# Kernel optimization log

Measured on AMD Instinct MI355X. Metric: run time of the kernel, lower is better.

The kernel has to match this reference:

```python
import jax, jax.numpy as jnp
import numpy as np

VOC, EDIM, HDIM, SSZ, SDIM, SDEPTH, PAD = 32000, 256, 256, 128, 128, 2, 0
N, BSZ = 64, 32
T = 2 * N - 1  # 127
N_ACTS = 2  # push, pop


def _linear(key, out_d, in_d):
    k1, k2 = jax.random.split(key)
    return (jax.random.normal(k1, (out_d, in_d), jnp.float32) * 0.02,
            jax.random.normal(k2, (out_d,), jnp.float32) * 0.02)


def setup_inputs() -> dict:
    key = jax.random.key(0)
    ks = jax.random.split(key, 9)
    emb_W = jax.random.normal(ks[0], (VOC, EDIM), jnp.float32) * 0.02
    emb_W = emb_W.at[PAD].set(0.0)  # padding_idx row is zero in torch
    W_e2h, b_e2h = _linear(ks[1], HDIM, EDIM)
    W_s2h, b_s2h = _linear(ks[2], HDIM, SDIM * SDEPTH)
    W_h2h, b_h2h = _linear(ks[3], HDIM, HDIM)
    W_h2i, b_h2i = _linear(ks[4], N_ACTS + 1, HDIM)
    W_h2s, b_h2s = _linear(ks[5], SDIM, HDIM)
    W_s2u, b_s2u = _linear(ks[6], SDIM, SDIM * SDEPTH)
    empty_elem = jax.random.normal(ks[7], (1, SDIM), jnp.float32) * 0.02
    inputs = jax.random.randint(ks[8], (N, BSZ), 0, VOC)
    return dict(inputs=inputs, emb_W=emb_W, W_e2h=W_e2h, b_e2h=b_e2h,
                W_s2h=W_s2h, b_s2h=b_s2h, W_h2h=W_h2h, b_h2h=b_h2h,
                W_h2i=W_h2i, b_h2i=b_h2i, W_h2s=W_h2s, b_h2s=b_h2s,
                W_s2u=W_s2u, b_s2u=b_s2u, empty_elem=empty_elem)


def _srnn(inputs, emb_W, W_e2h, b_e2h, W_s2h, b_s2h, W_h2h, b_h2h,
          W_h2i, b_h2i, W_h2s, b_h2s, W_s2u, b_s2u, empty_elem):
    bsz = inputs.shape[1]
    embs = emb_W[inputs]                                        # [N, bsz, edim]
    pads = jnp.broadcast_to(emb_W[PAD], (T - N, bsz, EDIM))     # padded tail
    buf0 = jnp.concatenate([embs, pads], axis=0)                # [T, bsz, edim]
    hid0 = jnp.zeros((bsz, HDIM), jnp.float32)
    stack0 = jnp.broadcast_to(empty_elem, (bsz, SSZ, SDIM))

    def step(carry, t):
        hid, stack, buf = carry
        tops = stack[:, :SDEPTH, :].reshape(bsz, SDEPTH * SDIM)
        inp = buf[t]                                            # [bsz, edim]
        ihid = inp @ W_e2h.T + b_e2h + tops @ W_s2h.T + b_s2h
        hid = jax.nn.relu(hid @ W_h2h.T + b_h2h + ihid)
        inst = ihid @ W_h2i.T + b_h2i                           # [bsz, 3]
        act = jax.nn.softmax(inst[:, :N_ACTS], axis=-1)
        gamma = 1.0 + jnp.log1p(jnp.exp(inst[:, N_ACTS:]))      # [bsz, 1]
        a = act ** gamma
        a = a / (jnp.sum(a, axis=-1, keepdims=True) + 1e-16)    # sharpened acts
        p_push, p_pop = a[:, :1], a[:, 1:]                      # [bsz, 1]
        # buffer update: pop shifts the whole buffer down one slot along time
        buf_pop = jnp.concatenate([jnp.zeros_like(buf[:1]), buf[:-1]], axis=0)
        buf = p_push[None] * buf + p_pop[None] * buf_pop        # [1,bsz,1] bcast
        push_val = jax.nn.relu(hid @ W_h2s.T + b_h2s)           # [bsz, sdim]
        u_val = jax.nn.relu(tops @ W_s2u.T + b_s2u)             # [bsz, sdim]
        z = jnp.zeros((bsz, 1, SDIM), jnp.float32)
        # W_push (shift down by 1) as an index roll
        stack_push = jnp.concatenate([z, stack[:, :-1, :]], axis=1)
        stack_push = stack_push.at[:, 0, :].add(push_val)
        # W_pop = shift up by SDEPTH, then W_push = shift down by 1
        up = jnp.concatenate([stack[:, SDEPTH:, :],
                              jnp.zeros((bsz, SDEPTH, SDIM), jnp.float32)], axis=1)
        stack_pop = jnp.concatenate([z, up[:, :-1, :]], axis=1)
        stack_pop = stack_pop.at[:, 0, :].add(u_val)
        stack_pop = stack_pop.at[:, SSZ - SDEPTH + 1:, :].add(empty_elem[0])
        stack = p_push[:, :, None] * stack_push + p_pop[:, :, None] * stack_pop
        return (hid, stack, buf), (hid, a, stack[:, 0, :])

    (hid, stack, _), (outputs, acts, top_elems) = jax.lax.scan(
        step, (hid0, stack0, buf0), jnp.arange(T))
    return outputs, hid, stack, acts, top_elems


def reference(inputs, emb_W, W_e2h, b_e2h, W_s2h, b_s2h, W_h2h, b_h2h,
              W_h2i, b_h2i, W_h2s, b_h2s, W_s2u, b_s2u, empty_elem):
    return _srnn(inputs, emb_W, W_e2h, b_e2h, W_s2h, b_s2h, W_h2h, b_h2h,
                 W_h2i, b_h2i, W_h2s, b_h2s, W_s2u, b_s2u, empty_elem)
```

## Files before the change

kernel.cpp:

```cpp
#include <hip/hip_runtime.h>
#include <stdint.h>
#include <math.h>


#define T_STEPS 127

#define OUT_OFF   0
#define HID_OFF   1040384
#define STACK_OFF 1048576
#define ACTS_OFF  1572864
#define TE_OFF    1580992

#define E2H_OFF_U 131072

typedef _Float16 h2 __attribute__((ext_vector_type(2)));

__device__ __forceinline__ unsigned packh2(float a, float b){
  h2 v; v.x = (_Float16)a; v.y = (_Float16)b;
  return __builtin_bit_cast(unsigned, v);
}
__device__ __forceinline__ float h2loF(unsigned u){ h2 v = __builtin_bit_cast(h2,u); return (float)v.x; }
__device__ __forceinline__ float h2hiF(unsigned u){ h2 v = __builtin_bit_cast(h2,u); return (float)v.y; }

#if __has_builtin(__builtin_amdgcn_fdot2)
__device__ __forceinline__ float fdot2(unsigned a, unsigned b, float c){
  return __builtin_amdgcn_fdot2(__builtin_bit_cast(h2,a), __builtin_bit_cast(h2,b), c, false);
}
#else
__device__ __forceinline__ float fdot2(unsigned a, unsigned b, float c){
  return c + h2loF(a)*h2loF(b) + h2hiF(a)*h2hiF(b);
}
#endif

#define CHOFF(u) (12*((u)>>3) + ((u)&7))

__global__ void prep_pack(const float* __restrict__ We2h, const float* __restrict__ Ws2h,
                          const float* __restrict__ Wh2h, const float* __restrict__ Wh2s,
                          const float* __restrict__ Ws2u, uint4* __restrict__ out4){
  int gid = blockIdx.x*256 + threadIdx.x;
  const float* src;
  if (gid < 16384){
    int i = gid >> 10, t_ = gid & 1023;
    const float* S = (t_ < 512) ? Ws2h : Wh2h;
    int r = t_ & 511, jp = r >> 2, ks = r & 3;
    int j = 2*jp + (i >> 3);
    int k0 = ks*64 + (i & 7)*8;
    src = S + j*256 + k0;
  } else if (gid < 20480){
    int l = gid - 16384, i = l >> 10, t_ = l & 1023;
    int jr = t_ >> 4, kb = t_ & 15;
    int j = 2*jr + (i >> 1);
    int k0 = kb*16 + (i & 1)*8;
    src = Wh2s + j*256 + k0;
  } else if (gid < 24576){
    int l = gid - 20480, i = l >> 10, t_ = l & 1023;
    int jr = t_ >> 4, kb = t_ & 15;
    int j = 2*jr + (i >> 1);
    int k0 = kb*16 + (i & 1)*8;
    src = Ws2u + j*256 + k0;
  } else {
    int l = gid - 24576;
    int i8 = l >> 8, j = l & 255;
    src = We2h + j*256 + i8*8;
  }
  uint4 r4;
  r4.x = packh2(src[0], src[1]); r4.y = packh2(src[2], src[3]);
  r4.z = packh2(src[4], src[5]); r4.w = packh2(src[6], src[7]);
  out4[gid] = r4;
}

__global__ void prep_e2h(const int* __restrict__ inputs, const float* __restrict__ embW,
                         const uint4* __restrict__ w04, unsigned* __restrict__ e2hpk){
  __shared__ float emb[8][256];
  int tid = threadIdx.x;
  int r2 = blockIdx.x >> 3, bg = blockIdx.x & 7;
  for (int q=0;q<8;q++){
    int rr = q >> 2, bb = q & 3;
    int tok = inputs[(2*r2+rr)*32 + bg*4+bb];
    emb[q][tid] = embW[tok*256 + tid];
  }
  __syncthreads();
  float acc[8] = {0.f,0.f,0.f,0.f,0.f,0.f,0.f,0.f};
  for (int i8=0;i8<32;i8++){
    uint4 u = w04[i8*256 + tid];
    unsigned uu[4] = {u.x,u.y,u.z,u.w};
    #pragma unroll
    for (int c=0;c<4;c++){
      float lo = h2loF(uu[c]), hi = h2hiF(uu[c]);
      int k = i8*8 + c*2;
      #pragma unroll
      for (int q=0;q<8;q++)
        acc[q] += emb[q][k]*lo + emb[q][k+1]*hi;
    }
  }
  int base = (bg*4)*8192 + r2*256 + tid;
  #pragma unroll
  for (int bb=0;bb<4;bb++)
    e2hpk[base + bb*8192] = packh2(acc[bb], acc[4+bb]);
}

__global__ __attribute__((amdgpu_flat_work_group_size(1024,1024), amdgpu_waves_per_eu(4,4)))
void srnn_main(const uint4* __restrict__ ws4, const unsigned* __restrict__ wsu,
               const float* __restrict__ b_e2h, const float* __restrict__ b_s2h,
               const float* __restrict__ b_h2h, const float* __restrict__ Wh2i,
               const float* __restrict__ b_h2i, const float* __restrict__ b_h2s,
               const float* __restrict__ b_s2u, const float* __restrict__ empty_el,
               float* __restrict__ out)
{
  __shared__ __align__(16) float    stk_s[128*128];
  __shared__ __align__(16) unsigned e2h_s[32*258];
  __shared__ __align__(16) unsigned s_pk[192];
  __shared__ __align__(16) unsigned hid_pk[192];
  __shared__ __align__(16) float    pv_s[128], uv_s[128];
  __shared__ __align__(16) float    accih[256], acchp[256];
  __shared__ __align__(16) float    emptyf_s[128];
  __shared__ float    wbuf[2][192];
  __shared__ unsigned pkwc[32];
  __shared__ float    partsum[12];
  __shared__ float    pp_s, pq_s;

  const int tid = threadIdx.x;
  const int b   = blockIdx.x;
  const int aside = tid >> 9;
  const int ar  = tid & 511;
  const int ajp = ar >> 2;
  const int aks = ar & 3;
  const int jr  = tid >> 4;
  const int ksb = tid & 15;
  const int g   = tid >> 6;
  const int cp  = tid & 63;

  uint4 w1r[16], w3r[4], w2r[4];
  #pragma unroll
  for (int i=0;i<16;i++) w1r[i] = ws4[i*1024 + tid];
  #pragma unroll
  for (int i=0;i<4;i++)  w3r[i] = ws4[16384 + i*1024 + tid];
  #pragma unroll
  for (int i=0;i<4;i++)  w2r[i] = ws4[20480 + i*1024 + tid];

  float bA0=0.f, bA1=0.f;
  if (aks==0){
    int j0 = 2*ajp;
    if (aside==0){ bA0 = b_e2h[j0]+b_s2h[j0]; bA1 = b_e2h[j0+1]+b_s2h[j0+1]; }
    else         { bA0 = b_h2h[j0];           bA1 = b_h2h[j0+1]; }
  }
  float bH0=0.f,bH1=0.f,bU0=0.f,bU1=0.f;
  if (ksb==0){ bH0=b_h2s[2*jr]; bH1=b_h2s[2*jr+1]; bU0=b_s2u[2*jr]; bU1=b_s2u[2*jr+1]; }
  float rW0=0.f,rW1=0.f,rW2=0.f;
  if (tid<256){ rW0=Wh2i[tid]; rW1=Wh2i[256+tid]; rW2=Wh2i[512+tid]; }
  const float bi0=b_h2i[0], bi1=b_h2i[1], bi2=b_h2i[2];

  const unsigned* e2hg = wsu + E2H_OFF_U + b*8192;
  #pragma unroll
  for (int q=0;q<8;q++){
    int idx = q*1024 + tid;
    e2h_s[(idx>>8)*258 + (idx&255)] = e2hg[idx];
  }
  {
    float2 e2 = *(const float2*)&empty_el[2*cp];
    #pragma unroll
    for (int j=0;j<8;j++)
      *(float2*)&stk_s[(8*g+j)*128 + 2*cp] = e2;
  }
  if (tid < 128){
    emptyf_s[tid] = empty_el[tid];
    hid_pk[CHOFF(tid)] = 0u;
    int cu = tid & 63;
    s_pk[CHOFF(tid)] = packh2(empty_el[2*cu], empty_el[2*cu+1]);
  }
  if (tid < 192){ wbuf[0][tid] = (tid==64)?1.f:0.f; wbuf[1][tid]=0.f; }
  if (tid < 32)  pkwc[tid] = (tid==0)? packh2(1.f,0.f) : 0u;
  __syncthreads();

  int cur = 0;
  for (int t=0;t<T_STEPS;++t){
    {
      const unsigned* act  = aside ? hid_pk : s_pk;
      const unsigned* actB = act + 48*aks;
      float x0 = 0.f, x1 = 0.f;
      if (aside==0){
        #pragma unroll
        for (int q=0;q<8;q++){
          int r2 = aks*8 + q;
          unsigned cw = pkwc[r2];
          uint2 e = *(const uint2*)&e2h_s[r2*258 + 2*ajp];
          x0 = fdot2(cw, e.x, x0);
          x1 = fdot2(cw, e.y, x1);
        }
      }
      #pragma unroll
      for (int i=0;i<8;i++){
        uint4 A  = *(const uint4*)(actB + 12*(i>>1) + 4*(i&1));
        uint4 Wa = w1r[i], Wb = w1r[8+i];
        x0 = fdot2(A.x,Wa.x,x0); x0 = fdot2(A.y,Wa.y,x0);
        x0 = fdot2(A.z,Wa.z,x0); x0 = fdot2(A.w,Wa.w,x0);
        x1 = fdot2(A.x,Wb.x,x1); x1 = fdot2(A.y,Wb.y,x1);
        x1 = fdot2(A.z,Wb.z,x1); x1 = fdot2(A.w,Wb.w,x1);
      }
      x0 += __shfl_xor(x0,1); x0 += __shfl_xor(x0,2);
      x1 += __shfl_xor(x1,1); x1 += __shfl_xor(x1,2);
      if (aks==0){
        float* dst = aside ? acchp : accih;
        *(float2*)&dst[2*ajp] = make_float2(x0 + bA0, x1 + bA1);
      }
    }
    __syncthreads();

    if (tid < 128){
      float2 ih2 = *(const float2*)&accih[2*tid];
      float2 hp2 = *(const float2*)&acchp[2*tid];
      float hn0 = fmaxf(ih2.x+hp2.x, 0.f);
      float hn1 = fmaxf(ih2.y+hp2.y, 0.f);
      hid_pk[CHOFF(tid)] = packh2(hn0,hn1);
      *(float2*)&out[OUT_OFF + t*8192 + b*256 + 2*tid] = make_float2(hn0,hn1);
      if (t==T_STEPS-1) *(float2*)&out[HID_OFF + b*256 + 2*tid] = make_float2(hn0,hn1);
    }
    if (tid < 256){
      float v = accih[tid];
      float p0=v*rW0, p1=v*rW1, p2=v*rW2;
      #pragma unroll
      for (int o=32;o>=1;o>>=1){ p0+=__shfl_xor(p0,o); p1+=__shfl_xor(p1,o); p2+=__shfl_xor(p2,o); }
      if ((tid&63)==0){ int w=tid>>6; partsum[w*3]=p0; partsum[w*3+1]=p1; partsum[w*3+2]=p2; }
    }
    __syncthreads();

    if (tid < 64){
      float i0 = bi0+partsum[0]+partsum[3]+partsum[6]+partsum[9];
      float i1 = bi1+partsum[1]+partsum[4]+partsum[7]+partsum[10];
      float gi = bi2+partsum[2]+partsum[5]+partsum[8]+partsum[11];
      float mx = fmaxf(i0,i1);
      float e0 = expf(i0-mx), e1 = expf(i1-mx);
      float inv = 1.f/(e0+e1);
      float act0 = e0*inv, act1 = e1*inv;
      float gamma = 1.f + log1pf(expf(gi));
      float A0 = powf(act0,gamma), A1 = powf(act1,gamma);
      float sden = A0+A1+1e-16f;
      float ppv = A0/sden, pqv = A1/sden;
      if (tid==0){
        pp_s = ppv; pq_s = pqv;
        *(float2*)&out[ACTS_OFF + t*64 + b*2] = make_float2(ppv,pqv);
      }
    }

    {
      const uint4* hptr = (const uint4*)(hid_pk + 12*ksb);
      const uint4* sptr = (const uint4*)(s_pk   + 12*ksb);
      uint4 H0 = hptr[0], H1 = hptr[1];
      uint4 S0 = sptr[0], S1 = sptr[1];
      float h0=0.f,h1=0.f,u0=0.f,u1=0.f;
      h0=fdot2(H0.x,w3r[0].x,h0); h0=fdot2(H0.y,w3r[0].y,h0); h0=fdot2(H0.z,w3r[0].z,h0); h0=fdot2(H0.w,w3r[0].w,h0);
      h0=fdot2(H1.x,w3r[1].x,h0); h0=fdot2(H1.y,w3r[1].y,h0); h0=fdot2(H1.z,w3r[1].z,h0); h0=fdot2(H1.w,w3r[1].w,h0);
      h1=fdot2(H0.x,w3r[2].x,h1); h1=fdot2(H0.y,w3r[2].y,h1); h1=fdot2(H0.z,w3r[2].z,h1); h1=fdot2(H0.w,w3r[2].w,h1);
      h1=fdot2(H1.x,w3r[3].x,h1); h1=fdot2(H1.y,w3r[3].y,h1); h1=fdot2(H1.z,w3r[3].z,h1); h1=fdot2(H1.w,w3r[3].w,h1);
      u0=fdot2(S0.x,w2r[0].x,u0); u0=fdot2(S0.y,w2r[0].y,u0); u0=fdot2(S0.z,w2r[0].z,u0); u0=fdot2(S0.w,w2r[0].w,u0);
      u0=fdot2(S1.x,w2r[1].x,u0); u0=fdot2(S1.y,w2r[1].y,u0); u0=fdot2(S1.z,w2r[1].z,u0); u0=fdot2(S1.w,w2r[1].w,u0);
      u1=fdot2(S0.x,w2r[2].x,u1); u1=fdot2(S0.y,w2r[2].y,u1); u1=fdot2(S0.z,w2r[2].z,u1); u1=fdot2(S0.w,w2r[2].w,u1);
      u1=fdot2(S1.x,w2r[3].x,u1); u1=fdot2(S1.y,w2r[3].y,u1); u1=fdot2(S1.z,w2r[3].z,u1); u1=fdot2(S1.w,w2r[3].w,u1);
      #pragma unroll
      for (int o=8;o>=1;o>>=1){
        h0+=__shfl_xor(h0,o); h1+=__shfl_xor(h1,o);
        u0+=__shfl_xor(u0,o); u1+=__shfl_xor(u1,o);
      }
      if (ksb==0){
        pv_s[2*jr]   = fmaxf(h0+bH0,0.f);
        pv_s[2*jr+1] = fmaxf(h1+bH1,0.f);
        uv_s[2*jr]   = fmaxf(u0+bU0,0.f);
        uv_s[2*jr+1] = fmaxf(u1+bU1,0.f);
      }
    }
    __syncthreads();
    const float pp = pp_s, pq = pq_s;

    {
      float2 w[10];
      #pragma unroll
      for (int k=0;k<10;k++){
        int r = 8*g - 1 + k;
        if (r >= 0 && r <= 127)
          w[k] = *(const float2*)&stk_s[r*128 + 2*cp];
      }
      if (g == 15) w[9] = *(const float2*)&emptyf_s[2*cp];
      float2 pv2 = make_float2(0.f,0.f), uv2 = make_float2(0.f,0.f);
      if (g == 0){ pv2 = *(const float2*)&pv_s[2*cp]; uv2 = *(const float2*)&uv_s[2*cp]; }
      float2 nn[8];
      #pragma unroll
      for (int j=0;j<8;j++){
        nn[j].x = pp*w[j].x + pq*w[j+2].x;
        nn[j].y = pp*w[j].y + pq*w[j+2].y;
      }
      if (g == 0){
        nn[0].x = pp*pv2.x + pq*uv2.x;
        nn[0].y = pp*pv2.y + pq*uv2.y;
      }
      if (tid < 128){
        int k = 64+tid;
        wbuf[cur^1][k] = pp*wbuf[cur][k] + pq*wbuf[cur][k-1];
      } else if (tid < 160){
        int r2 = tid-128;
        int k1 = 65 + t - 2*r2;
        float wa = wbuf[cur][k1], wb2 = wbuf[cur][k1-1], wc2 = wbuf[cur][k1-2];
        pkwc[r2] = packh2(pp*wa+pq*wb2, pp*wb2+pq*wc2);
      }
      __syncthreads();
      #pragma unroll
      for (int j=0;j<8;j++)
        *(float2*)&stk_s[(8*g+j)*128 + 2*cp] = nn[j];
      if (g == 0){
        *(float2*)&out[TE_OFF + t*4096 + b*128 + 2*cp] = nn[0];
        s_pk[CHOFF(cp)]      = packh2(nn[0].x, nn[0].y);
        s_pk[CHOFF(64+cp)]   = packh2(nn[1].x, nn[1].y);
      }
    }
    __syncthreads();
    cur ^= 1;
  }

  #pragma unroll
  for (int j=0;j<8;j++){
    int r = 8*g + j;
    *(float2*)&out[STACK_OFF + b*16384 + r*128 + 2*cp] =
      *(const float2*)&stk_s[r*128 + 2*cp];
  }
}

extern "C" void kernel_launch(void* const* d_in, const int* in_sizes, int n_in,
                              void* d_out, int out_size, void* d_ws, size_t ws_size,
                              hipStream_t stream){
  const int*   inputs = (const int*)d_in[0];
  const float* embW   = (const float*)d_in[1];
  const float* We2h   = (const float*)d_in[2];
  const float* b_e2h  = (const float*)d_in[3];
  const float* Ws2h   = (const float*)d_in[4];
  const float* b_s2h  = (const float*)d_in[5];
  const float* Wh2h   = (const float*)d_in[6];
  const float* b_h2h  = (const float*)d_in[7];
  const float* Wh2i   = (const float*)d_in[8];
  const float* b_h2i  = (const float*)d_in[9];
  const float* Wh2s   = (const float*)d_in[10];
  const float* b_h2s  = (const float*)d_in[11];
  const float* Ws2u   = (const float*)d_in[12];
  const float* b_s2u  = (const float*)d_in[13];
  const float* empty  = (const float*)d_in[14];
  unsigned* wsu = (unsigned*)d_ws;

  prep_pack<<<dim3(128), dim3(256), 0, stream>>>(We2h, Ws2h, Wh2h, Wh2s, Ws2u, (uint4*)wsu);
  prep_e2h<<<dim3(256), dim3(256), 0, stream>>>(inputs, embW, ((const uint4*)wsu)+24576, wsu + E2H_OFF_U);
  srnn_main<<<dim3(32), dim3(1024), 0, stream>>>((const uint4*)wsu, (const unsigned*)wsu,
                                                 b_e2h, b_s2h, b_h2h, Wh2i, b_h2i,
                                                 b_h2s, b_s2u, empty, (float*)d_out);
}
```

Measured before the change: 896.4 us.

## Halve block to 512 threads with more weights in registers per thread

The main recurrent kernel now runs with 512 threads per block instead of 1024. Each thread keeps twice as many packed fp16 weights in registers and does a longer dot-product chain with fewer shuffle reductions. The h2s and s2u projections are split across two thread halves, the weight packing layout is rewritten to match, and the padded CHOFF activation layout is dropped. The aim is to cut per-step barrier and shuffle cost in the serial 127-step loop, at the cost of higher register pressure and less parallelism per step.

```diff
diff --git a/kernel.cpp b/kernel.cpp
--- a/kernel.cpp
+++ b/kernel.cpp
@@ -31,8 +31,6 @@
   return c + h2loF(a)*h2loF(b) + h2hiF(a)*h2hiF(b);
 }
 #endif
-
-#define CHOFF(u) (12*((u)>>3) + ((u)&7))
 
 __global__ void prep_pack(const float* __restrict__ We2h, const float* __restrict__ Ws2h,
                           const float* __restrict__ Wh2h, const float* __restrict__ Wh2s,
@@ -40,24 +38,22 @@
   int gid = blockIdx.x*256 + threadIdx.x;
   const float* src;
   if (gid < 16384){
-    int i = gid >> 10, t_ = gid & 1023;
-    const float* S = (t_ < 512) ? Ws2h : Wh2h;
-    int r = t_ & 511, jp = r >> 2, ks = r & 3;
-    int j = 2*jp + (i >> 3);
-    int k0 = ks*64 + (i & 7)*8;
+    int i = gid >> 9, t_ = gid & 511;
+    int aside = t_ >> 8, ar = t_ & 255;
+    const float* S = aside ? Wh2h : Ws2h;
+    int ajp = ar >> 1, aks = ar & 1;
+    int j  = 2*ajp + (i >> 4);
+    int k0 = aks*128 + (i & 15)*8;
     src = S + j*256 + k0;
-  } else if (gid < 20480){
-    int l = gid - 16384, i = l >> 10, t_ = l & 1023;
-    int jr = t_ >> 4, kb = t_ & 15;
-    int j = 2*jr + (i >> 1);
-    int k0 = kb*16 + (i & 1)*8;
-    src = Wh2s + j*256 + k0;
   } else if (gid < 24576){
-    int l = gid - 20480, i = l >> 10, t_ = l & 1023;
-    int jr = t_ >> 4, kb = t_ & 15;
-    int j = 2*jr + (i >> 1);
-    int k0 = kb*16 + (i & 1)*8;
-    src = Ws2u + j*256 + k0;
+    int l = gid - 16384;
+    int i = l >> 9, t_ = l & 511;
+    int hside = t_ >> 8, r = t_ & 255;
+    const float* S = hside ? Ws2u : Wh2s;
+    int jr = r >> 2, ksb = r & 3;
+    int j  = 2*jr + (i >> 3);
+    int k0 = ksb*64 + (i & 7)*8;
+    src = S + j*256 + k0;
   } else {
     int l = gid - 24576;
     int i8 = l >> 8, j = l & 255;
@@ -99,7 +95,7 @@
     e2hpk[base + bb*8192] = packh2(acc[bb], acc[4+bb]);
 }
 
-__global__ __attribute__((amdgpu_flat_work_group_size(1024,1024), amdgpu_waves_per_eu(4,4)))
+__global__ __attribute__((amdgpu_flat_work_group_size(512,512), amdgpu_waves_per_eu(2,2)))
 void srnn_main(const uint4* __restrict__ ws4, const unsigned* __restrict__ wsu,
                const float* __restrict__ b_e2h, const float* __restrict__ b_s2h,
                const float* __restrict__ b_h2h, const float* __restrict__ Wh2i,
@@ -109,8 +105,8 @@
 {
   __shared__ __align__(16) float    stk_s[128*128];
   __shared__ __align__(16) unsigned e2h_s[32*258];
-  __shared__ __align__(16) unsigned s_pk[192];
-  __shared__ __align__(16) unsigned hid_pk[192];
+  __shared__ __align__(16) unsigned s_pk[128];
+  __shared__ __align__(16) unsigned hid_pk[128];
   __shared__ __align__(16) float    pv_s[128], uv_s[128];
   __shared__ __align__(16) float    accih[256], acchp[256];
   __shared__ __align__(16) float    emptyf_s[128];
@@ -121,22 +117,22 @@
 
   const int tid = threadIdx.x;
   const int b   = blockIdx.x;
-  const int aside = tid >> 9;
-  const int ar  = tid & 511;
-  const int ajp = ar >> 2;
-  const int aks = ar & 3;
-  const int jr  = tid >> 4;
-  const int ksb = tid & 15;
+  const int aside = tid >> 8;
+  const int ar  = tid & 255;
+  const int ajp = ar >> 1;
+  const int aks = ar & 1;
+  const int hside = tid >> 8;
+  const int r   = tid & 255;
+  const int jr  = r >> 2;
+  const int ksb = r & 3;
   const int g   = tid >> 6;
   const int cp  = tid & 63;
 
-  uint4 w1r[16], w3r[4], w2r[4];
-  #pragma unroll
-  for (int i=0;i<16;i++) w1r[i] = ws4[i*1024 + tid];
-  #pragma unroll
-  for (int i=0;i<4;i++)  w3r[i] = ws4[16384 + i*1024 + tid];
-  #pragma unroll
-  for (int i=0;i<4;i++)  w2r[i] = ws4[20480 + i*1024 + tid];
+  uint4 w1r[32], w23r[16];
+  #pragma unroll
+  for (int i=0;i<32;i++) w1r[i]  = ws4[i*512 + tid];
+  #pragma unroll
+  for (int i=0;i<16;i++) w23r[i] = ws4[16384 + i*512 + tid];
 
   float bA0=0.f, bA1=0.f;
   if (aks==0){
@@ -144,29 +140,32 @@
     if (aside==0){ bA0 = b_e2h[j0]+b_s2h[j0]; bA1 = b_e2h[j0+1]+b_s2h[j0+1]; }
     else         { bA0 = b_h2h[j0];           bA1 = b_h2h[j0+1]; }
   }
-  float bH0=0.f,bH1=0.f,bU0=0.f,bU1=0.f;
-  if (ksb==0){ bH0=b_h2s[2*jr]; bH1=b_h2s[2*jr+1]; bU0=b_s2u[2*jr]; bU1=b_s2u[2*jr+1]; }
+  float bB0=0.f, bB1=0.f;
+  if (ksb==0){
+    const float* bb = hside ? b_s2u : b_h2s;
+    bB0 = bb[2*jr]; bB1 = bb[2*jr+1];
+  }
   float rW0=0.f,rW1=0.f,rW2=0.f;
   if (tid<256){ rW0=Wh2i[tid]; rW1=Wh2i[256+tid]; rW2=Wh2i[512+tid]; }
   const float bi0=b_h2i[0], bi1=b_h2i[1], bi2=b_h2i[2];
 
   const unsigned* e2hg = wsu + E2H_OFF_U + b*8192;
   #pragma unroll
-  for (int q=0;q<8;q++){
-    int idx = q*1024 + tid;
+  for (int q=0;q<16;q++){
+    int idx = q*512 + tid;
     e2h_s[(idx>>8)*258 + (idx&255)] = e2hg[idx];
   }
   {
     float2 e2 = *(const float2*)&empty_el[2*cp];
     #pragma unroll
-    for (int j=0;j<8;j++)
-      *(float2*)&stk_s[(8*g+j)*128 + 2*cp] = e2;
+    for (int j=0;j<16;j++)
+      *(float2*)&stk_s[(16*g+j)*128 + 2*cp] = e2;
   }
   if (tid < 128){
     emptyf_s[tid] = empty_el[tid];
-    hid_pk[CHOFF(tid)] = 0u;
+    hid_pk[tid] = 0u;
     int cu = tid & 63;
-    s_pk[CHOFF(tid)] = packh2(empty_el[2*cu], empty_el[2*cu+1]);
+    s_pk[tid] = packh2(empty_el[2*cu], empty_el[2*cu+1]);
   }
   if (tid < 192){ wbuf[0][tid] = (tid==64)?1.f:0.f; wbuf[1][tid]=0.f; }
   if (tid < 32)  pkwc[tid] = (tid==0)? packh2(1.f,0.f) : 0u;
@@ -175,30 +174,29 @@
   int cur = 0;
   for (int t=0;t<T_STEPS;++t){
     {
-      const unsigned* act  = aside ? hid_pk : s_pk;
-      const unsigned* actB = act + 48*aks;
+      const uint4* act4 = ((const uint4*)(aside ? hid_pk : s_pk)) + aks*16;
       float x0 = 0.f, x1 = 0.f;
       if (aside==0){
-        #pragma unroll
-        for (int q=0;q<8;q++){
-          int r2 = aks*8 + q;
+        #pragma unroll 4
+        for (int q=0;q<16;q++){
+          int r2 = aks*16 + q;
           unsigned cw = pkwc[r2];
           uint2 e = *(const uint2*)&e2h_s[r2*258 + 2*ajp];
           x0 = fdot2(cw, e.x, x0);
           x1 = fdot2(cw, e.y, x1);
         }
       }
-      #pragma unroll
-      for (int i=0;i<8;i++){
-        uint4 A  = *(const uint4*)(actB + 12*(i>>1) + 4*(i&1));
-        uint4 Wa = w1r[i], Wb = w1r[8+i];
+      #pragma unroll 4
+      for (int i=0;i<16;i++){
+        uint4 A  = act4[i];
+        uint4 Wa = w1r[i], Wb = w1r[16+i];
         x0 = fdot2(A.x,Wa.x,x0); x0 = fdot2(A.y,Wa.y,x0);
         x0 = fdot2(A.z,Wa.z,x0); x0 = fdot2(A.w,Wa.w,x0);
         x1 = fdot2(A.x,Wb.x,x1); x1 = fdot2(A.y,Wb.y,x1);
         x1 = fdot2(A.z,Wb.z,x1); x1 = fdot2(A.w,Wb.w,x1);
       }
-      x0 += __shfl_xor(x0,1); x0 += __shfl_xor(x0,2);
-      x1 += __shfl_xor(x1,1); x1 += __shfl_xor(x1,2);
+      x0 += __shfl_xor(x0,1);
+      x1 += __shfl_xor(x1,1);
       if (aks==0){
         float* dst = aside ? acchp : accih;
         *(float2*)&dst[2*ajp] = make_float2(x0 + bA0, x1 + bA1);
@@ -211,7 +209,7 @@
       float2 hp2 = *(const float2*)&acchp[2*tid];
       float hn0 = fmaxf(ih2.x+hp2.x, 0.f);
       float hn1 = fmaxf(ih2.y+hp2.y, 0.f);
-      hid_pk[CHOFF(tid)] = packh2(hn0,hn1);
+      hid_pk[tid] = packh2(hn0,hn1);
       *(float2*)&out[OUT_OFF + t*8192 + b*256 + 2*tid] = make_float2(hn0,hn1);
       if (t==T_STEPS-1) *(float2*)&out[HID_OFF + b*256 + 2*tid] = make_float2(hn0,hn1);
     }
@@ -243,55 +241,38 @@
     }
 
     {
-      const uint4* hptr = (const uint4*)(hid_pk + 12*ksb);
-      const uint4* sptr = (const uint4*)(s_pk   + 12*ksb);
-      uint4 H0 = hptr[0], H1 = hptr[1];
-      uint4 S0 = sptr[0], S1 = sptr[1];
-      float h0=0.f,h1=0.f,u0=0.f,u1=0.f;
-      h0=fdot2(H0.x,w3r[0].x,h0); h0=fdot2(H0.y,w3r[0].y,h0); h0=fdot2(H0.z,w3r[0].z,h0); h0=fdot2(H0.w,w3r[0].w,h0);
-      h0=fdot2(H1.x,w3r[1].x,h0); h0=fdot2(H1.y,w3r[1].y,h0); h0=fdot2(H1.z,w3r[1].z,h0); h0=fdot2(H1.w,w3r[1].w,h0);
-      h1=fdot2(H0.x,w3r[2].x,h1); h1=fdot2(H0.y,w3r[2].y,h1); h1=fdot2(H0.z,w3r[2].z,h1); h1=fdot2(H0.w,w3r[2].w,h1);
-      h1=fdot2(H1.x,w3r[3].x,h1); h1=fdot2(H1.y,w3r[3].y,h1); h1=fdot2(H1.z,w3r[3].z,h1); h1=fdot2(H1.w,w3r[3].w,h1);
-      u0=fdot2(S0.x,w2r[0].x,u0); u0=fdot2(S0.y,w2r[0].y,u0); u0=fdot2(S0.z,w2r[0].z,u0); u0=fdot2(S0.w,w2r[0].w,u0);
-      u0=fdot2(S1.x,w2r[1].x,u0); u0=fdot2(S1.y,w2r[1].y,u0); u0=fdot2(S1.z,w2r[1].z,u0); u0=fdot2(S1.w,w2r[1].w,u0);
-      u1=fdot2(S0.x,w2r[2].x,u1); u1=fdot2(S0.y,w2r[2].y,u1); u1=fdot2(S0.z,w2r[2].z,u1); u1=fdot2(S0.w,w2r[2].w,u1);
-      u1=fdot2(S1.x,w2r[3].x,u1); u1=fdot2(S1.y,w2r[3].y,u1); u1=fdot2(S1.z,w2r[3].z,u1); u1=fdot2(S1.w,w2r[3].w,u1);
-      #pragma unroll
-      for (int o=8;o>=1;o>>=1){
-        h0+=__shfl_xor(h0,o); h1+=__shfl_xor(h1,o);
-        u0+=__shfl_xor(u0,o); u1+=__shfl_xor(u1,o);
-      }
+      const uint4* act4b = ((const uint4*)(hside ? s_pk : hid_pk)) + ksb*8;
+      float y0 = 0.f, y1 = 0.f;
+      #pragma unroll 4
+      for (int i=0;i<8;i++){
+        uint4 A  = act4b[i];
+        uint4 Wa = w23r[i], Wb = w23r[8+i];
+        y0 = fdot2(A.x,Wa.x,y0); y0 = fdot2(A.y,Wa.y,y0);
+        y0 = fdot2(A.z,Wa.z,y0); y0 = fdot2(A.w,Wa.w,y0);
+        y1 = fdot2(A.x,Wb.x,y1); y1 = fdot2(A.y,Wb.y,y1);
+        y1 = fdot2(A.z,Wb.z,y1); y1 = fdot2(A.w,Wb.w,y1);
+      }
+      y0 += __shfl_xor(y0,1); y0 += __shfl_xor(y0,2);
+      y1 += __shfl_xor(y1,1); y1 += __shfl_xor(y1,2);
       if (ksb==0){
-        pv_s[2*jr]   = fmaxf(h0+bH0,0.f);
-        pv_s[2*jr+1] = fmaxf(h1+bH1,0.f);
-        uv_s[2*jr]   = fmaxf(u0+bU0,0.f);
-        uv_s[2*jr+1] = fmaxf(u1+bU1,0.f);
+        float* dst = hside ? uv_s : pv_s;
+        *(float2*)&dst[2*jr] = make_float2(fmaxf(y0+bB0,0.f), fmaxf(y1+bB1,0.f));
       }
     }
     __syncthreads();
     const float pp = pp_s, pq = pq_s;
 
     {
-      float2 w[10];
-      #pragma unroll
-      for (int k=0;k<10;k++){
-        int r = 8*g - 1 + k;
-        if (r >= 0 && r <= 127)
-          w[k] = *(const float2*)&stk_s[r*128 + 2*cp];
-      }
-      if (g == 15) w[9] = *(const float2*)&emptyf_s[2*cp];
+      float2 w[18];
+      #pragma unroll
+      for (int k=0;k<18;k++){
+        int rr = 16*g - 1 + k;
+        if (rr >= 0 && rr <= 127)
+          w[k] = *(const float2*)&stk_s[rr*128 + 2*cp];
+      }
+      if (g == 7) w[17] = *(const float2*)&emptyf_s[2*cp];
       float2 pv2 = make_float2(0.f,0.f), uv2 = make_float2(0.f,0.f);
       if (g == 0){ pv2 = *(const float2*)&pv_s[2*cp]; uv2 = *(const float2*)&uv_s[2*cp]; }
-      float2 nn[8];
-      #pragma unroll
-      for (int j=0;j<8;j++){
-        nn[j].x = pp*w[j].x + pq*w[j+2].x;
-        nn[j].y = pp*w[j].y + pq*w[j+2].y;
-      }
-      if (g == 0){
-        nn[0].x = pp*pv2.x + pq*uv2.x;
-        nn[0].y = pp*pv2.y + pq*uv2.y;
-      }
       if (tid < 128){
         int k = 64+tid;
         wbuf[cur^1][k] = pp*wbuf[cur][k] + pq*wbuf[cur][k-1];
@@ -303,12 +284,21 @@
       }
       __syncthreads();
       #pragma unroll
-      for (int j=0;j<8;j++)
-        *(float2*)&stk_s[(8*g+j)*128 + 2*cp] = nn[j];
+      for (int j=0;j<16;j++){
+        w[j].x = pp*w[j].x + pq*w[j+2].x;
+        w[j].y = pp*w[j].y + pq*w[j+2].y;
+      }
       if (g == 0){
-        *(float2*)&out[TE_OFF + t*4096 + b*128 + 2*cp] = nn[0];
-        s_pk[CHOFF(cp)]      = packh2(nn[0].x, nn[0].y);
-        s_pk[CHOFF(64+cp)]   = packh2(nn[1].x, nn[1].y);
+        w[0].x = pp*pv2.x + pq*uv2.x;
+        w[0].y = pp*pv2.y + pq*uv2.y;
+      }
+      #pragma unroll
+      for (int j=0;j<16;j++)
+        *(float2*)&stk_s[(16*g+j)*128 + 2*cp] = w[j];
+      if (g == 0){
+        *(float2*)&out[TE_OFF + t*4096 + b*128 + 2*cp] = w[0];
+        s_pk[cp]    = packh2(w[0].x, w[0].y);
+        s_pk[64+cp] = packh2(w[1].x, w[1].y);
       }
     }
     __syncthreads();
@@ -316,10 +306,10 @@
   }
 
   #pragma unroll
-  for (int j=0;j<8;j++){
-    int r = 8*g + j;
-    *(float2*)&out[STACK_OFF + b*16384 + r*128 + 2*cp] =
-      *(const float2*)&stk_s[r*128 + 2*cp];
+  for (int j=0;j<16;j++){
+    int rr = 16*g + j;
+    *(float2*)&out[STACK_OFF + b*16384 + rr*128 + 2*cp] =
+      *(const float2*)&stk_s[rr*128 + 2*cp];
   }
 }
 
@@ -345,7 +335,7 @@
 
   prep_pack<<<dim3(128), dim3(256), 0, stream>>>(We2h, Ws2h, Wh2h, Wh2s, Ws2u, (uint4*)wsu);
   prep_e2h<<<dim3(256), dim3(256), 0, stream>>>(inputs, embW, ((const uint4*)wsu)+24576, wsu + E2H_OFF_U);
-  srnn_main<<<dim3(32), dim3(1024), 0, stream>>>((const uint4*)wsu, (const unsigned*)wsu,
-                                                 b_e2h, b_s2h, b_h2h, Wh2i, b_h2i,
-                                                 b_h2s, b_s2u, empty, (float*)d_out);
-}
+  srnn_main<<<dim3(32), dim3(512), 0, stream>>>((const uint4*)wsu, (const unsigned*)wsu,
+                                                b_e2h, b_s2h, b_h2h, Wh2i, b_h2i,
+                                                b_h2s, b_s2u, empty, (float*)d_out);
+}
```

Result: slower. 1.658 ms (+84.9%).
